# Kernel tuning notes

Hardware: AMD Instinct MI355X
Metric: run time of the kernel (lower is better)

The kernel has to match this reference:

```python
import jax, jax.numpy as jnp
import numpy as np

LAMBDA = 0.7
RATIO = 3
EPS = 1e-6


def setup_inputs() -> dict:
    key = jax.random.key(0)
    k1, k2, k3 = jax.random.split(key, 3)
    bs, n, w, h = 8, 7, 640, 640
    preds = jax.random.normal(k1, (bs, n, w, h), dtype=jnp.float32)
    labels = jax.random.randint(k2, (bs, n, w, h), 0, 2, dtype=jnp.int32)
    training_mask = jax.random.randint(k3, (bs, w, h), 0, 2, dtype=jnp.int32)
    return {"preds": preds, "labels": labels, "training_mask": training_mask}


def _dice(S, G):
    # S, G: [C, P]; per-channel dice coefficient, then mean over channels
    num = 2.0 * jnp.sum(S * G, axis=-1)
    den = jnp.sum(S * S, axis=-1) + jnp.sum(G * G, axis=-1) + EPS
    return jnp.mean(num / den)


def _single_sample(pred, label, mask):
    # pred, label: [n, P]; mask: [P]
    P = pred.shape[-1]
    p = jax.nn.sigmoid(pred)
    pred_n = p[-1] * mask            # masked full-text prediction
    label_n = label[-1] * mask

    # --- OHEM mask M (cal_M): keep all positives + top (ratio*n_pos) hardest negatives ---
    pos = pred_n >= 0.5
    n_pos = jnp.sum(pos)
    n_neg_all = jnp.sum(~pos)
    k = n_pos * RATIO
    # sigmoid outputs are in (0,1); sentinel -1 pushes positives to the end of the descending sort
    neg_vals = jnp.where(pos, -1.0, pred_n)
    sorted_desc = -jnp.sort(-neg_vals)
    thr = sorted_desc[jnp.clip(k - 1, 0, P - 1)]  # k-th largest negative score
    ohem_active = (n_neg_all > k) & (k > 0)
    M = jnp.where(ohem_active, (pred_n >= thr).astype(jnp.float32), 1.0)

    # L_c: dice loss on OHEM-selected full-text map
    L_c = 1.0 - _dice((pred_n * M)[None, :], (label_n * M)[None, :])

    # L_s: dice loss on shrunk kernels, gated by predicted text region W
    W = (pred_n >= 0.5).astype(jnp.float32)
    L_s = 1.0 - _dice(p[:-1] * W, label[:-1] * W)

    loss = LAMBDA * L_c + (1.0 - LAMBDA) * L_s
    return L_c, L_s, loss


def reference(preds, labels, training_mask):
    bs, n, w, h = preds.shape
    preds = preds.reshape(bs, n, w * h)
    labels = labels.reshape(bs, n, w * h).astype(jnp.float32)
    mask = training_mask.reshape(bs, w * h).astype(jnp.float32)
    L_c, L_s, loss = jax.vmap(_single_sample)(preds, labels, mask)
    # reduction='mean'
    return L_c.mean(), L_s.mean(), loss.mean()
```

## Files before the change

kernel.cpp:

```cpp
#include <hip/hip_runtime.h>

#define BS   8
#define NCH  7
#define PX   409600
#define PBLK 400
#define EPSF 1e-6f

__device__ __forceinline__ float sigf(float x) {
    return __builtin_amdgcn_rcpf(1.0f + __expf(-x));
}

__device__ __forceinline__ unsigned wred_u(unsigned v) {
    #pragma unroll
    for (int o = 32; o; o >>= 1) v += __shfl_down(v, o);
    return v;
}

__device__ __forceinline__ float wred_f(float v) {
    #pragma unroll
    for (int o = 32; o; o >>= 1) v += __shfl_down(v, o);
    return v;
}


__global__ __launch_bounds__(256, 4) void k_fat(const float* __restrict__ preds,
                                                const int* __restrict__ labels,
                                                const int* __restrict__ mask,
                                                unsigned* __restrict__ n_pos,
                                                unsigned* __restrict__ n_nz,
                                                float* __restrict__ sums) {
    int b = blockIdx.y;
    int base = (blockIdx.x * 256 + threadIdx.x) * 4;
    const float* pr = preds + (size_t)b * NCH * PX;
    const int*   lb = labels + (size_t)b * NCH * PX;
    const int*   mk = mask + (size_t)b * PX;

    int4   m4 = *(const int4*)(mk + base);
    float4 p[7];
    int4   l[7];
    #pragma unroll
    for (int c = 0; c < 7; c++) {
        p[c] = *(const float4*)(pr + c * PX + base);
        l[c] = *(const int4*)(lb + c * PX + base);
    }

    float ms[4] = {(float)m4.x, (float)m4.y, (float)m4.z, (float)m4.w};
    float p6[4] = {p[6].x, p[6].y, p[6].z, p[6].w};
    float l6[4] = {(float)l[6].x, (float)l[6].y, (float)l[6].z, (float)l[6].w};

    unsigned pos = 0, nz = 0;
    float a0 = 0.f, a1 = 0.f, a2 = 0.f;
    float W[4];
    #pragma unroll
    for (int u = 0; u < 4; u++) {
        float pn = sigf(p6[u]) * ms[u];
        bool P = (pn >= 0.5f);
        pos += P;
        nz  += (!P && __float_as_uint(pn) != 0u);
        W[u] = P ? 1.0f : 0.0f;
        float ln = l6[u] * ms[u];
        a0 += pn * ln;
        a1 += pn * pn;
        a2 += ln;
    }

    float acc[18];
    #pragma unroll
    for (int j = 0; j < 18; j++) acc[j] = 0.f;
    #pragma unroll
    for (int c = 0; c < 6; c++) {
        float ps[4] = {p[c].x, p[c].y, p[c].z, p[c].w};
        float ls[4] = {(float)l[c].x, (float)l[c].y, (float)l[c].z, (float)l[c].w};
        #pragma unroll
        for (int u = 0; u < 4; u++) {
            float s = sigf(ps[u]);
            float lw = ls[u] * W[u];
            acc[c]      += s * lw;
            acc[6 + c]  += s * s * W[u];
            acc[12 + c] += lw;
        }
    }

    __shared__ float red[4][21];
    __shared__ unsigned ws2[2][4];
    int lane = threadIdx.x & 63, wid = threadIdx.x >> 6;
    {
        float v = wred_f(a0); if (lane == 0) red[wid][18] = v;
        v = wred_f(a1);       if (lane == 0) red[wid][19] = v;
        v = wred_f(a2);       if (lane == 0) red[wid][20] = v;
    }
    #pragma unroll
    for (int j = 0; j < 18; j++) {
        float v = wred_f(acc[j]);
        if (lane == 0) red[wid][j] = v;
    }
    unsigned pv = wred_u(pos), zv = wred_u(nz);
    if (lane == 0) { ws2[0][wid] = pv; ws2[1][wid] = zv; }
    __syncthreads();
    if (threadIdx.x < 21) {
        float tot = red[0][threadIdx.x] + red[1][threadIdx.x] +
                    red[2][threadIdx.x] + red[3][threadIdx.x];
        int j = threadIdx.x;
        int idx = (j < 18) ? (((size_t)b * 7 + (j % 6)) * 3 + (j / 6))
                           : (((size_t)b * 7 + 6) * 3 + (j - 18));
        atomicAdd(&sums[idx], tot);
    }
    if (threadIdx.x == 64) {
        unsigned pt = ws2[0][0] + ws2[0][1] + ws2[0][2] + ws2[0][3];
        unsigned zt = ws2[1][0] + ws2[1][1] + ws2[1][2] + ws2[1][3];
        if (pt) atomicAdd(&n_pos[b], pt);
        if (zt) atomicAdd(&n_nz[b], zt);
    }
}

__global__ __launch_bounds__(256) void k_final(const float* __restrict__ preds,
                                               const int* __restrict__ labels,
                                               const int* __restrict__ mask,
                                               const unsigned* __restrict__ n_pos,
                                               const unsigned* __restrict__ n_nz,
                                               const float* __restrict__ sums,
                                               float* __restrict__ out) {
    __shared__ float fr[BS * 21];
    if (threadIdx.x < BS * 21) fr[threadIdx.x] = sums[threadIdx.x];
    __syncthreads();

    __shared__ unsigned hist[256];
    __shared__ unsigned sh_sel, sh_rem;
    __shared__ float red[4][3];

    for (int b = 0; b < BS; b++) {
        unsigned np_ = n_pos[b];
        unsigned k = np_ * 3u;
        unsigned nneg = (unsigned)PX - np_;
        bool active = (nneg > k) && (k > 0u);
        if (!active || k > n_nz[b]) continue;

        const float* pr = preds + ((size_t)b * NCH + 6) * PX;
        const int*   lb = labels + ((size_t)b * NCH + 6) * PX;
        const int*   mk = mask + (size_t)b * PX;
        unsigned prefix = 0u, krem = k;
        const unsigned masks[4] = {0x00000000u, 0xFF000000u, 0xFFFF0000u, 0xFFFFFF00u};
        for (int lv = 0; lv < 4; lv++) {
            int shift = 24 - 8 * lv;
            unsigned msk = masks[lv];
            hist[threadIdx.x] = 0u;
            __syncthreads();
            for (int g = threadIdx.x; g < PX / 4; g += 256) {
                int px = g * 4;
                float4 p4 = *(const float4*)(pr + px);
                int4   m4 = *(const int4*)(mk + px);
                float pa[4] = {p4.x, p4.y, p4.z, p4.w};
                float mm[4] = {(float)m4.x, (float)m4.y, (float)m4.z, (float)m4.w};
                #pragma unroll
                for (int u = 0; u < 4; u++) {
                    float pn = sigf(pa[u]) * mm[u];
                    if (pn < 0.5f) {
                        unsigned bits = __float_as_uint(pn);
                        if ((bits & msk) == prefix)
                            atomicAdd(&hist[(bits >> shift) & 0xFFu], 1u);
                    }
                }
            }
            __syncthreads();
            if (threadIdx.x == 0) {
                unsigned acc = 0, rem = krem, sel = 0;
                for (int i = 255; i >= 0; i--) {
                    acc += hist[i];
                    if (acc >= krem) { sel = (unsigned)i; rem = krem - (acc - hist[i]); break; }
                }
                sh_sel = sel; sh_rem = rem;
            }
            __syncthreads();
            prefix |= (sh_sel << shift);
            krem = sh_rem;
            __syncthreads();
        }
        float thr = __uint_as_float(prefix);

        float a0 = 0.f, a1 = 0.f, a2 = 0.f;
        for (int g = threadIdx.x; g < PX / 4; g += 256) {
            int px = g * 4;
            float4 p4 = *(const float4*)(pr + px);
            int4   l4 = *(const int4*)(lb + px);
            int4   m4 = *(const int4*)(mk + px);
            float pa[4] = {p4.x, p4.y, p4.z, p4.w};
            float la[4] = {(float)l4.x, (float)l4.y, (float)l4.z, (float)l4.w};
            float mm[4] = {(float)m4.x, (float)m4.y, (float)m4.z, (float)m4.w};
            #pragma unroll
            for (int u = 0; u < 4; u++) {
                float pn = sigf(pa[u]) * mm[u];
                float Mi = (pn >= thr) ? 1.0f : 0.0f;
                float ln = la[u] * mm[u];
                a0 += pn * ln * Mi;
                a1 += pn * pn * Mi;
                a2 += ln * Mi;
            }
        }
        int lane = threadIdx.x & 63, wid = threadIdx.x >> 6;
        float v0 = wred_f(a0), v1 = wred_f(a1), v2 = wred_f(a2);
        if (lane == 0) { red[wid][0] = v0; red[wid][1] = v1; red[wid][2] = v2; }
        __syncthreads();
        if (threadIdx.x < 3) {
            fr[(b * 7 + 6) * 3 + threadIdx.x] =
                red[0][threadIdx.x] + red[1][threadIdx.x] +
                red[2][threadIdx.x] + red[3][threadIdx.x];
        }
        __syncthreads();
    }

    if (threadIdx.x == 0) {
        float Lc = 0.f, Ls = 0.f;
        #pragma unroll
        for (int b = 0; b < BS; b++) {
            const float* s6 = fr + (b * 7 + 6) * 3;
            Lc += 1.0f - (2.0f * s6[0]) / (s6[1] + s6[2] + EPSF);
            float acc = 0.f;
            #pragma unroll
            for (int c = 0; c < 6; c++) {
                const float* sc = fr + (b * 7 + c) * 3;
                acc += (2.0f * sc[0]) / (sc[1] + sc[2] + EPSF);
            }
            Ls += 1.0f - acc * (1.0f / 6.0f);
        }
        float lc_m = Lc * (1.0f / (float)BS);
        float ls_m = Ls * (1.0f / (float)BS);
        out[0] = lc_m;
        out[1] = ls_m;
        out[2] = 0.7f * lc_m + 0.3f * ls_m;
    }
}

extern "C" void kernel_launch(void* const* d_in, const int* in_sizes, int n_in,
                              void* d_out, int out_size, void* d_ws, size_t ws_size,
                              hipStream_t stream) {
    const float* preds = (const float*)d_in[0];
    const int* labels  = (const int*)d_in[1];
    const int* mask    = (const int*)d_in[2];
    float* out = (float*)d_out;

    unsigned* n_pos = (unsigned*)d_ws;
    unsigned* n_nz  = n_pos + BS;
    float*    sums  = (float*)(n_nz + BS);

    hipMemsetAsync(d_ws, 0, (2 * BS + BS * 21) * sizeof(unsigned), stream);

    hipLaunchKernelGGL(k_fat, dim3(PBLK, BS), dim3(256), 0, stream,
                       preds, labels, mask, n_pos, n_nz, sums);

    hipLaunchKernelGGL(k_final, dim3(1), dim3(256), 0, stream,
                       preds, labels, mask, n_pos, n_nz, sums, out);
}
```

Baseline: 237.5 us.

## Make reduction kernel persistent-style with register double-buffered loads

The main reduction kernel now launches fewer blocks (160 per sample instead of 400), and each thread handles five strided iterations of 2-wide vectors instead of a single 4-wide chunk. The next iteration's loads are issued into a second register buffer before the current one is computed, so memory latency overlaps with sigmoid and accumulation work. This cuts the per-block reduction and atomic overhead and improves latency hiding. In exchange it uses narrower 8-byte loads and more registers, which may lower occupancy under the launch bound.

New measurement: 293.1 us. +23.4%, slower.

```diff
diff --git a/kernel.cpp b/kernel.cpp
--- a/kernel.cpp
+++ b/kernel.cpp
@@ -1,10 +1,11 @@
 #include <hip/hip_runtime.h>
 
-#define BS   8
-#define NCH  7
-#define PX   409600
-#define PBLK 400
-#define EPSF 1e-6f
+#define BS    8
+#define NCH   7
+#define PX    409600
+#define SBLK  160
+#define ITER  5
+#define EPSF  1e-6f
 
 __device__ __forceinline__ float sigf(float x) {
     return __builtin_amdgcn_rcpf(1.0f + __expf(-x));
@@ -30,69 +31,90 @@
                                                 unsigned* __restrict__ n_nz,
                                                 float* __restrict__ sums) {
     int b = blockIdx.y;
-    int base = (blockIdx.x * 256 + threadIdx.x) * 4;
     const float* pr = preds + (size_t)b * NCH * PX;
     const int*   lb = labels + (size_t)b * NCH * PX;
     const int*   mk = mask + (size_t)b * PX;
 
-    int4   m4 = *(const int4*)(mk + base);
-    float4 p[7];
-    int4   l[7];
+    unsigned pos = 0, nz = 0;
+    float accC[3] = {0.f, 0.f, 0.f};
+    float acc[18];
+    #pragma unroll
+    for (int j = 0; j < 18; j++) acc[j] = 0.f;
+
+    float2 curf[8], nxtf[8];
+    int2   curi[8], nxti[8];
+
+    const int istride = SBLK * 256 * 2;
+    int base = (blockIdx.x * 256 + threadIdx.x) * 2;
+
+    curi[0] = *(const int2*)(mk + base);
     #pragma unroll
     for (int c = 0; c < 7; c++) {
-        p[c] = *(const float4*)(pr + c * PX + base);
-        l[c] = *(const int4*)(lb + c * PX + base);
-    }
-
-    float ms[4] = {(float)m4.x, (float)m4.y, (float)m4.z, (float)m4.w};
-    float p6[4] = {p[6].x, p[6].y, p[6].z, p[6].w};
-    float l6[4] = {(float)l[6].x, (float)l[6].y, (float)l[6].z, (float)l[6].w};
-
-    unsigned pos = 0, nz = 0;
-    float a0 = 0.f, a1 = 0.f, a2 = 0.f;
-    float W[4];
-    #pragma unroll
-    for (int u = 0; u < 4; u++) {
-        float pn = sigf(p6[u]) * ms[u];
-        bool P = (pn >= 0.5f);
-        pos += P;
-        nz  += (!P && __float_as_uint(pn) != 0u);
-        W[u] = P ? 1.0f : 0.0f;
-        float ln = l6[u] * ms[u];
-        a0 += pn * ln;
-        a1 += pn * pn;
-        a2 += ln;
-    }
-
-    float acc[18];
-    #pragma unroll
-    for (int j = 0; j < 18; j++) acc[j] = 0.f;
-    #pragma unroll
-    for (int c = 0; c < 6; c++) {
-        float ps[4] = {p[c].x, p[c].y, p[c].z, p[c].w};
-        float ls[4] = {(float)l[c].x, (float)l[c].y, (float)l[c].z, (float)l[c].w};
+        curf[1 + c] = *(const float2*)(pr + c * PX + base);
+        curi[1 + c] = *(const int2*)(lb + c * PX + base);
+    }
+
+    #pragma unroll
+    for (int it = 0; it < ITER; it++) {
+        if (it + 1 < ITER) {
+            int nb = base + istride;
+            nxti[0] = *(const int2*)(mk + nb);
+            #pragma unroll
+            for (int c = 0; c < 7; c++) {
+                nxtf[1 + c] = *(const float2*)(pr + c * PX + nb);
+                nxti[1 + c] = *(const int2*)(lb + c * PX + nb);
+            }
+        }
+
+        float ms[2] = {(float)curi[0].x, (float)curi[0].y};
+        float p6[2] = {curf[7].x, curf[7].y};
+        float l6[2] = {(float)curi[7].x, (float)curi[7].y};
+        float W[2];
         #pragma unroll
-        for (int u = 0; u < 4; u++) {
-            float s = sigf(ps[u]);
-            float lw = ls[u] * W[u];
-            acc[c]      += s * lw;
-            acc[6 + c]  += s * s * W[u];
-            acc[12 + c] += lw;
+        for (int u = 0; u < 2; u++) {
+            float pn = sigf(p6[u]) * ms[u];
+            bool P = (pn >= 0.5f);
+            pos += P;
+            nz  += (!P && __float_as_uint(pn) != 0u);
+            W[u] = P ? 1.0f : 0.0f;
+            float ln = l6[u] * ms[u];
+            accC[0] += pn * ln;
+            accC[1] += pn * pn;
+            accC[2] += ln;
+        }
+        #pragma unroll
+        for (int c = 0; c < 6; c++) {
+            float ps[2] = {curf[1 + c].x, curf[1 + c].y};
+            float ls[2] = {(float)curi[1 + c].x, (float)curi[1 + c].y};
+            #pragma unroll
+            for (int u = 0; u < 2; u++) {
+                float s = sigf(ps[u]);
+                float lw = ls[u] * W[u];
+                acc[c]      += s * lw;
+                acc[6 + c]  += s * s * W[u];
+                acc[12 + c] += lw;
+            }
+        }
+
+        if (it + 1 < ITER) {
+            #pragma unroll
+            for (int j = 0; j < 8; j++) { curf[j] = nxtf[j]; curi[j] = nxti[j]; }
+            base += istride;
         }
     }
 
     __shared__ float red[4][21];
     __shared__ unsigned ws2[2][4];
     int lane = threadIdx.x & 63, wid = threadIdx.x >> 6;
-    {
-        float v = wred_f(a0); if (lane == 0) red[wid][18] = v;
-        v = wred_f(a1);       if (lane == 0) red[wid][19] = v;
-        v = wred_f(a2);       if (lane == 0) red[wid][20] = v;
-    }
     #pragma unroll
     for (int j = 0; j < 18; j++) {
         float v = wred_f(acc[j]);
         if (lane == 0) red[wid][j] = v;
+    }
+    #pragma unroll
+    for (int j = 0; j < 3; j++) {
+        float v = wred_f(accC[j]);
+        if (lane == 0) red[wid][18 + j] = v;
     }
     unsigned pv = wred_u(pos), zv = wred_u(nz);
     if (lane == 0) { ws2[0][wid] = pv; ws2[1][wid] = zv; }
@@ -244,7 +266,7 @@
 
     hipMemsetAsync(d_ws, 0, (2 * BS + BS * 21) * sizeof(unsigned), stream);
 
-    hipLaunchKernelGGL(k_fat, dim3(PBLK, BS), dim3(256), 0, stream,
+    hipLaunchKernelGGL(k_fat, dim3(SBLK, BS), dim3(256), 0, stream,
                        preds, labels, mask, n_pos, n_nz, sums);
 
     hipLaunchKernelGGL(k_final, dim3(1), dim3(256), 0, stream,
```
